# Performance work log

Hardware: AMD Instinct MI355X
Metric: run time of the kernel (lower is better)

Reference implementation:

```python
import jax, jax.numpy as jnp
import numpy as np
from jax import lax

DIM = 1024      # model dim
DS = 16         # d_state
DC = 4          # d_conv
EXP = 2
DI = DIM * EXP  # d_inner = 2048
B, L = 2, 1024


def setup_inputs() -> dict:
    key = jax.random.key(0)
    ks = jax.random.split(key, 10)
    s = lambda k, shape, sc: jax.random.normal(k, shape, jnp.float32) * sc
    return {
        "x": s(ks[0], (B, L, DIM), 1.0),
        "norm_w": jnp.ones((DIM,), jnp.float32),
        "norm_b": jnp.zeros((DIM,), jnp.float32),
        "in_proj_w": s(ks[1], (2 * DI, DIM), DIM ** -0.5),
        "conv_w": s(ks[2], (DI, 1, DC), DC ** -0.5),   # depthwise: (out=DI, in/groups=1, K)
        "conv_b": jnp.zeros((DI,), jnp.float32),
        "x_proj_w": s(ks[3], (2 * DS + 1, DI), DI ** -0.5),
        "dt_w": s(ks[4], (DI, 1), 1.0),
        "dt_b": jax.random.uniform(ks[5], (DI,), jnp.float32, -0.001, 0.001),
        "A_log": s(ks[6], (DI, DS), 1.0),              # self.A (randn); A = -exp(A_log)
        "D_skip": jnp.ones((DI,), jnp.float32),
        "out_proj_w": s(ks[7], (DIM, DI), DI ** -0.5),
    }


def _ssm(x, x_proj_w, dt_w, dt_b, A_log, D_skip):
    # x: (B, L, DI)
    xp = jnp.einsum('bli,pi->blp', x, x_proj_w)            # (B, L, 2*DS+1)
    delta = jax.nn.softplus(xp[..., :1] * dt_w[:, 0] + dt_b)  # (B, L, DI)
    Bp = xp[..., 1:DS + 1]                                  # (B, L, DS)
    Cp = xp[..., DS + 1:]                                   # (B, L, DS)
    A = -jnp.exp(A_log)                                     # (DI, DS)
    dA = jnp.exp(delta[..., None] * A)                      # (B, L, DI, DS)
    dB = delta[..., None] * Bp[:, :, None, :] * x[..., None]  # (B, L, DI, DS)

    def step(h, inp):
        dA_t, dB_t, C_t = inp                               # (B,DI,DS),(B,DI,DS),(B,DS)
        h = dA_t * h + dB_t
        return h, jnp.einsum('bdn,bn->bd', h, C_t)

    h0 = jnp.zeros((x.shape[0], DI, DS), x.dtype)
    _, ys = lax.scan(step, h0, (jnp.swapaxes(dA, 0, 1),
                                jnp.swapaxes(dB, 0, 1),
                                jnp.swapaxes(Cp, 0, 1)))
    y = jnp.swapaxes(ys, 0, 1)                              # (B, L, DI)
    return y + x * D_skip


def reference(x, norm_w, norm_b, in_proj_w, conv_w, conv_b,
              x_proj_w, dt_w, dt_b, A_log, D_skip, out_proj_w):
    # LayerNorm
    mu = x.mean(-1, keepdims=True)
    var = ((x - mu) ** 2).mean(-1, keepdims=True)
    xn = (x - mu) * lax.rsqrt(var + 1e-5) * norm_w + norm_b
    # input projection and gate split
    xz = jnp.einsum('bld,pd->blp', xn, in_proj_w)           # (B, L, 2*DI)
    xi, z = xz[..., :DI], xz[..., DI:]
    # causal depthwise conv (torch pads K-1 both sides then slices [:L] == left-pad K-1)
    xc = lax.conv_general_dilated(jnp.swapaxes(xi, 1, 2), conv_w, (1,),
                                  [(DC - 1, 0)], feature_group_count=DI,
                                  dimension_numbers=('NCH', 'OIH', 'NCH'))
    xc = jnp.swapaxes(xc + conv_b[None, :, None], 1, 2)     # (B, L, DI)
    xc = jax.nn.silu(xc)
    y = _ssm(xc, x_proj_w, dt_w, dt_b, A_log, D_skip)
    y = y * jax.nn.silu(z)
    return x + jnp.einsum('bli,di->bld', y, out_proj_w)
```

## Files before the change

kernel.cpp:

```cpp
#include <hip/hip_runtime.h>
#include <stdint.h>

#define BATCH 2
#define SEQ   1024
#define DIM_  1024
#define DS_   16
#define DI_   2048
#define NTOK  (BATCH*SEQ)
#define NSEG  32
#define LSEG  (SEQ/NSEG)

typedef unsigned short u16;
using s16x8 = __attribute__((ext_vector_type(8))) short;
using f32x4 = __attribute__((ext_vector_type(4))) float;
using u16x4 = __attribute__((ext_vector_type(4))) unsigned short;
using u16x8 = __attribute__((ext_vector_type(8))) unsigned short;

__device__ __forceinline__ float bf2f(u16 u) {
  union { unsigned int i; float f; } c; c.i = ((unsigned int)u) << 16; return c.f;
}
__device__ __forceinline__ u16 f2bf(float f) {
  union { float f; unsigned int i; } c; c.f = f;
  unsigned int r = c.i + 0x7fffu + ((c.i >> 16) & 1u);
  return (u16)(r >> 16);
}
__device__ __forceinline__ float softplus_f(float x) {
  return (x > 15.f) ? x : __logf(1.f + __expf(x));
}
__device__ __forceinline__ u16x4 f4_to_bf(float4 v) {
  u16x4 r; r[0] = f2bf(v.x); r[1] = f2bf(v.y); r[2] = f2bf(v.z); r[3] = f2bf(v.w);
  return r;
}

#define N4_INW  (2 * DI_ * DIM_ / 4)
#define N4_OUTW (DIM_ * DI_ / 4)
__global__ __launch_bounds__(256) void cvt_all_kernel(const float* __restrict__ in_w,
    const float* __restrict__ out_w, const float* __restrict__ xproj_w,
    u16* __restrict__ in_w_bf, u16* __restrict__ out_w_bf, u16* __restrict__ xpw_bf) {
  int i = blockIdx.x * 256 + threadIdx.x;
  if (i < N4_INW) {
    ((u16x4*)in_w_bf)[i] = f4_to_bf(((const float4*)in_w)[i]);
  } else if (i < N4_INW + N4_OUTW) {
    int j = i - N4_INW;
    ((u16x4*)out_w_bf)[j] = f4_to_bf(((const float4*)out_w)[j]);
  } else {
    int j = i - (N4_INW + N4_OUTW);
    if (j >= 32768) return;
    int p = (j * 4) >> 11;
    u16x4 r;
    if (p < 33) r = f4_to_bf(((const float4*)xproj_w)[j]);
    else { r[0] = 0; r[1] = 0; r[2] = 0; r[3] = 0; }
    ((u16x4*)xpw_bf)[j] = r;
  }
}

__global__ __launch_bounds__(256) void ln_kernel(const float* __restrict__ x,
    const float* __restrict__ w, const float* __restrict__ b, u16* __restrict__ xn) {
  int t = blockIdx.x, tid = threadIdx.x;
  const float* row = x + (size_t)t * DIM_;
  float4 v = ((const float4*)row)[tid];
  float f[4] = {v.x, v.y, v.z, v.w};
  float s = 0.f, sq = 0.f;
#pragma unroll
  for (int j = 0; j < 4; j++) { s += f[j]; sq += f[j] * f[j]; }
#pragma unroll
  for (int m = 1; m < 64; m <<= 1) { s += __shfl_xor(s, m); sq += __shfl_xor(sq, m); }
  __shared__ float rs_[4], rq_[4];
  int wv = tid >> 6;
  if ((tid & 63) == 0) { rs_[wv] = s; rq_[wv] = sq; }
  __syncthreads();
  s = rs_[0] + rs_[1] + rs_[2] + rs_[3];
  sq = rq_[0] + rq_[1] + rq_[2] + rq_[3];
  float mu = s * (1.0f / DIM_);
  float var = sq * (1.0f / DIM_) - mu * mu;
  float rstd = rsqrtf(var + 1e-5f);
  float4 wn = ((const float4*)w)[tid];
  float4 bn = ((const float4*)b)[tid];
  u16x4 o;
  o[0] = f2bf((f[0] - mu) * rstd * wn.x + bn.x);
  o[1] = f2bf((f[1] - mu) * rstd * wn.y + bn.y);
  o[2] = f2bf((f[2] - mu) * rstd * wn.z + bn.z);
  o[3] = f2bf((f[3] - mu) * rstd * wn.w + bn.w);
  *(u16x4*)(xn + (size_t)t * DIM_ + tid * 4) = o;
}

template<int TBM, int TBN, int BK, typename OUT, int EPI, int KSPLIT = 1, int SWZ = 0>
__global__ __launch_bounds__(256) void gemm_bt(const u16* __restrict__ A,
    const u16* __restrict__ Wt, OUT* __restrict__ C, const float* __restrict__ X,
    int M, int N, int K) {
  constexpr int LDT = BK + 8;
  constexpr int TPR = BK / 8;
  constexpr int RPP = 256 / TPR;
  constexpr int ALn = TBM / RPP;
  constexpr int BLn = TBN / RPP;
  constexpr int KK = BK / 32;
  constexpr int WM = TBM / 2, WN = TBN / 2;
  constexpr int MI = WM / 16, NJ = WN / 16;
  __shared__ __align__(16) u16 sA[TBM * LDT];
  __shared__ __align__(16) u16 sB[TBN * LDT];
  const int tid = threadIdx.x;
  const int lane = tid & 63, wv = tid >> 6;
  const int wm = (wv >> 1) * WM, wn = (wv & 1) * WN;
  const int bxl = SWZ ? ((blockIdx.x & 7) * (gridDim.x >> 3) + (blockIdx.x >> 3))
                      : blockIdx.x;
  const int bm0 = blockIdx.y * TBM, bn0 = bxl * TBN;
  const int q = lane >> 4, r16 = lane & 15;
  const int srow = tid / TPR, scol = (tid % TPR) * 8;
  const int kc = K / KSPLIT;
  const int k0 = (KSPLIT > 1) ? blockIdx.z * kc : 0;
  const int kend = k0 + kc;

  f32x4 acc[MI][NJ];
#pragma unroll
  for (int i = 0; i < MI; i++)
#pragma unroll
    for (int j = 0; j < NJ; j++)
#pragma unroll
      for (int r = 0; r < 4; r++) acc[i][j][r] = 0.f;

  const u16* Ag = A + (size_t)bm0 * K + scol + k0;
  const u16* Wg = Wt + (size_t)bn0 * K + scol + k0;
  s16x8 ra[ALn], rb[BLn];
#pragma unroll
  for (int i = 0; i < ALn; i++) ra[i] = *(const s16x8*)(Ag + (size_t)(srow + i * RPP) * K);
#pragma unroll
  for (int i = 0; i < BLn; i++) rb[i] = *(const s16x8*)(Wg + (size_t)(srow + i * RPP) * K);

  for (int kt = k0; kt < kend; kt += BK) {
    __syncthreads();
#pragma unroll
    for (int i = 0; i < ALn; i++) *(s16x8*)&sA[(srow + i * RPP) * LDT + scol] = ra[i];
#pragma unroll
    for (int i = 0; i < BLn; i++) *(s16x8*)&sB[(srow + i * RPP) * LDT + scol] = rb[i];
    __syncthreads();
    int kn = kt + BK - k0;
    if (kn < kc) {
#pragma unroll
      for (int i = 0; i < ALn; i++) ra[i] = *(const s16x8*)(Ag + (size_t)(srow + i * RPP) * K + kn);
#pragma unroll
      for (int i = 0; i < BLn; i++) rb[i] = *(const s16x8*)(Wg + (size_t)(srow + i * RPP) * K + kn);
    }
#pragma unroll
    for (int kk = 0; kk < KK; kk++) {
      s16x8 fa[MI], fb[NJ];
#pragma unroll
      for (int i = 0; i < MI; i++)
        fa[i] = *(const s16x8*)&sA[(wm + i * 16 + r16) * LDT + kk * 32 + q * 8];
#pragma unroll
      for (int j = 0; j < NJ; j++)
        fb[j] = *(const s16x8*)&sB[(wn + j * 16 + r16) * LDT + kk * 32 + q * 8];
#pragma unroll
      for (int i = 0; i < MI; i++)
#pragma unroll
        for (int j = 0; j < NJ; j++)
          acc[i][j] = __builtin_amdgcn_mfma_f32_16x16x32_bf16(fa[i], fb[j], acc[i][j], 0, 0, 0);
    }
  }
  OUT* Cz = C + ((KSPLIT > 1) ? (size_t)blockIdx.z * M * N : 0);
#pragma unroll
  for (int i = 0; i < MI; i++)
#pragma unroll
    for (int j = 0; j < NJ; j++) {
      int row0 = bm0 + wm + i * 16 + q * 4;
      int col = bn0 + wn + j * 16 + r16;
#pragma unroll
      for (int r = 0; r < 4; r++) {
        size_t off = (size_t)(row0 + r) * N + col;
        float v = acc[i][j][r];
        if constexpr (EPI == 1) v += X[off];
        if constexpr (sizeof(OUT) == 2) Cz[off] = f2bf(v);
        else                            Cz[off] = v;
      }
    }
}

__global__ __launch_bounds__(256) void conv_silu_kernel(const u16* __restrict__ xz,
    const float* __restrict__ cw, const float* __restrict__ cb, u16* __restrict__ xc) {
  int t = blockIdx.x;
  int l = t & (SEQ - 1);
  int c0 = threadIdx.x * 8;
  float acc[8], wk[8][4];
#pragma unroll
  for (int j = 0; j < 8; j++) {
    float4 wv = ((const float4*)cw)[c0 + j];
    wk[j][0] = wv.x; wk[j][1] = wv.y; wk[j][2] = wv.z; wk[j][3] = wv.w;
    acc[j] = cb[c0 + j];
  }
#pragma unroll
  for (int k = 0; k < 4; k++) {
    int lk = l - 3 + k;
    if (lk >= 0) {
      u16x8 v = *(const u16x8*)(xz + (size_t)(t - 3 + k) * (2 * DI_) + c0);
#pragma unroll
      for (int j = 0; j < 8; j++) acc[j] = fmaf(bf2f(v[j]), wk[j][k], acc[j]);
    }
  }
  u16x8 o;
#pragma unroll
  for (int j = 0; j < 8; j++) {
    float a = acc[j];
    o[j] = f2bf(a / (1.0f + __expf(-a)));
  }
  *(u16x8*)(xc + (size_t)t * DI_ + c0) = o;
}

__global__ __launch_bounds__(256) void xp_finish_kernel(const float* __restrict__ part,
    const float* __restrict__ dtw, const float* __restrict__ dtb,
    u16* __restrict__ xz, float* __restrict__ bc) {
  int t = blockIdx.x;
  int tid = threadIdx.x;
  __shared__ float xps[64];
  if (tid < 64) {
    float s = 0.f;
#pragma unroll
    for (int k = 0; k < 8; k++)
      s += part[(size_t)k * NTOK * 64 + (size_t)t * 64 + tid];
    xps[tid] = s;
  }
  __syncthreads();
  if (tid < 32) bc[(size_t)t * 32 + tid] = xps[1 + tid];
  float dr = xps[0];
  int c0 = tid * 8;
  float wv[8], bv[8];
  *(float4*)wv = ((const float4*)(dtw + c0))[0];
  *(float4*)(wv + 4) = ((const float4*)(dtw + c0))[1];
  *(float4*)bv = ((const float4*)(dtb + c0))[0];
  *(float4*)(bv + 4) = ((const float4*)(dtb + c0))[1];
  u16x8 o;
#pragma unroll
  for (int j = 0; j < 8; j++) o[j] = f2bf(softplus_f(dr * wv[j] + bv[j]));
  *(u16x8*)(xz + (size_t)t * (2 * DI_) + c0) = o;
}

__global__ __launch_bounds__(256) void scan_pass1(const float* __restrict__ bc,
    const u16* __restrict__ dlt, const u16* __restrict__ xc,
    const float* __restrict__ A_log, float* __restrict__ P, float* __restrict__ Q) {
  int tid = threadIdx.x;
  int lane = tid & 63, wv = tid >> 6;
  int nl = (lane & 3) * 4;
  int d = blockIdx.x * 64 + wv * 16 + (lane >> 2);
  int s = blockIdx.y, b = blockIdx.z;
  int t0 = b * SEQ + s * LSEG;
  float4 Ain = *(const float4*)(A_log + d * DS_ + nl);
  f32x4 Av;
  Av[0] = -__expf(Ain.x); Av[1] = -__expf(Ain.y);
  Av[2] = -__expf(Ain.z); Av[3] = -__expf(Ain.w);
  f32x4 Pv, h;
#pragma unroll
  for (int i = 0; i < 4; i++) { Pv[i] = 1.f; h[i] = 0.f; }
#pragma unroll 8
  for (int j = 0; j < LSEG; j++) {
    int t = t0 + j;
    float delta = bf2f(dlt[(size_t)t * (2 * DI_) + d]);
    float xcv = bf2f(xc[(size_t)t * DI_ + d]);
    float4 B4 = *(const float4*)(bc + (size_t)t * 32 + nl);
    float du = delta * xcv;
#pragma unroll
    for (int i = 0; i < 4; i++) {
      float a = __expf(delta * Av[i]);
      Pv[i] *= a;
      float bi = (i == 0) ? B4.x : (i == 1) ? B4.y : (i == 2) ? B4.z : B4.w;
      h[i] = fmaf(a, h[i], du * bi);
    }
  }
  size_t idx = ((size_t)((b * NSEG + s) * DI_ + d)) * 16 + nl;
  *(f32x4*)(P + idx) = Pv;
  *(f32x4*)(Q + idx) = h;
}

__global__ __launch_bounds__(256) void scan_combine(const float* __restrict__ P,
    float* __restrict__ Q) {
  int g = blockIdx.x * 256 + threadIdx.x;
  int n = g & 15, d = (g >> 4) & (DI_ - 1), b = g >> 15;
  size_t base = ((size_t)b * NSEG * DI_ + d) * 16 + n;
  constexpr size_t STR = (size_t)DI_ * 16;
  float p_[NSEG], q_[NSEG];
#pragma unroll
  for (int s = 0; s < NSEG; s++) {
    p_[s] = P[base + s * STR];
    q_[s] = Q[base + s * STR];
  }
  float hh = 0.f;
#pragma unroll
  for (int s = 0; s < NSEG; s++) {
    Q[base + s * STR] = hh;
    hh = fmaf(p_[s], hh, q_[s]);
  }
}

__global__ __launch_bounds__(256) void scan_pass2(const float* __restrict__ bc,
    const u16* __restrict__ dlt, const u16* __restrict__ xc,
    const float* __restrict__ A_log, const float* __restrict__ Dskip,
    const float* __restrict__ Hin, u16* __restrict__ yb) {
  int tid = threadIdx.x;
  int lane = tid & 63, wv = tid >> 6;
  int nl = (lane & 3) * 4;
  int d = blockIdx.x * 64 + wv * 16 + (lane >> 2);
  int s = blockIdx.y, b = blockIdx.z;
  int t0 = b * SEQ + s * LSEG;
  float4 Ain = *(const float4*)(A_log + d * DS_ + nl);
  f32x4 Av;
  Av[0] = -__expf(Ain.x); Av[1] = -__expf(Ain.y);
  Av[2] = -__expf(Ain.z); Av[3] = -__expf(Ain.w);
  float Dv = Dskip[d];
  size_t idx = ((size_t)((b * NSEG + s) * DI_ + d)) * 16 + nl;
  f32x4 h = *(const f32x4*)(Hin + idx);
#pragma unroll 8
  for (int j = 0; j < LSEG; j++) {
    int t = t0 + j;
    float delta = bf2f(dlt[(size_t)t * (2 * DI_) + d]);
    float xcv = bf2f(xc[(size_t)t * DI_ + d]);
    float4 B4 = *(const float4*)(bc + (size_t)t * 32 + nl);
    float4 C4 = *(const float4*)(bc + (size_t)t * 32 + 16 + nl);
    float du = delta * xcv;
#pragma unroll
    for (int i = 0; i < 4; i++) {
      float a = __expf(delta * Av[i]);
      float bi = (i == 0) ? B4.x : (i == 1) ? B4.y : (i == 2) ? B4.z : B4.w;
      h[i] = fmaf(a, h[i], du * bi);
    }
    float p = h[0] * C4.x;
    p = fmaf(h[1], C4.y, p);
    p = fmaf(h[2], C4.z, p);
    p = fmaf(h[3], C4.w, p);
    p += __shfl_xor(p, 1);
    p += __shfl_xor(p, 2);
    if ((lane & 3) == 0) {
      float z = bf2f(dlt[(size_t)t * (2 * DI_) + DI_ + d]);
      float sz = z / (1.0f + __expf(-z));
      yb[(size_t)t * DI_ + d] = f2bf((p + xcv * Dv) * sz);
    }
  }
}

extern "C" void kernel_launch(void* const* d_in, const int* in_sizes, int n_in,
                              void* d_out, int out_size, void* d_ws, size_t ws_size,
                              hipStream_t stream) {
  const float* x      = (const float*)d_in[0];
  const float* norm_w = (const float*)d_in[1];
  const float* norm_b = (const float*)d_in[2];
  const float* in_w   = (const float*)d_in[3];
  const float* conv_w = (const float*)d_in[4];
  const float* conv_b = (const float*)d_in[5];
  const float* xproj_w= (const float*)d_in[6];
  const float* dt_w   = (const float*)d_in[7];
  const float* dt_b   = (const float*)d_in[8];
  const float* A_log  = (const float*)d_in[9];
  const float* D_skip = (const float*)d_in[10];
  const float* out_w  = (const float*)d_in[11];
  float* out = (float*)d_out;

  char* ws = (char*)d_ws;
  size_t off = 0;
  auto alloc = [&](size_t bytes) { void* p = ws + off; off += (bytes + 255) & ~255ULL; return p; };
  u16* in_w_bf  = (u16*)alloc((size_t)2 * DI_ * DIM_ * 2);
  u16* out_w_bf = (u16*)alloc((size_t)DIM_ * DI_ * 2);
  u16* xpw_bf   = (u16*)alloc((size_t)64 * DI_ * 2);
  u16* xn       = (u16*)alloc((size_t)NTOK * DIM_ * 2);
  u16* xz       = (u16*)alloc((size_t)NTOK * 2 * DI_ * 2);
  u16* xc       = (u16*)alloc((size_t)NTOK * DI_ * 2);
  float* bc     = (float*)alloc((size_t)NTOK * 32 * 4);
  float* xp_part= (float*)alloc((size_t)8 * NTOK * 64 * 4);
  float* P      = (float*)alloc((size_t)BATCH * NSEG * DI_ * 16 * 4);
  float* Q      = (float*)alloc((size_t)BATCH * NSEG * DI_ * 16 * 4);
  u16* yb       = (u16*)alloc((size_t)NTOK * DI_ * 2);

  cvt_all_kernel<<<(N4_INW + N4_OUTW + 32768 + 255) / 256, 256, 0, stream>>>(
      in_w, out_w, xproj_w, in_w_bf, out_w_bf, xpw_bf);
  ln_kernel<<<NTOK, 256, 0, stream>>>(x, norm_w, norm_b, xn);
  gemm_bt<128, 128, 64, u16, 0, 1, 1><<<dim3((2 * DI_) / 128, NTOK / 128), 256, 0, stream>>>(
      xn, in_w_bf, xz, nullptr, NTOK, 2 * DI_, DIM_);
  conv_silu_kernel<<<NTOK, 256, 0, stream>>>(xz, conv_w, conv_b, xc);
  gemm_bt<64, 64, 32, float, 0, 8><<<dim3(1, NTOK / 64, 8), 256, 0, stream>>>(
      xc, xpw_bf, xp_part, nullptr, NTOK, 64, DI_);
  xp_finish_kernel<<<NTOK, 256, 0, stream>>>(xp_part, dt_w, dt_b, xz, bc);
  scan_pass1<<<dim3(DI_ / 64, NSEG, BATCH), 256, 0, stream>>>(bc, xz, xc, A_log, P, Q);
  scan_combine<<<BATCH * DI_ * 16 / 256, 256, 0, stream>>>(P, Q);
  scan_pass2<<<dim3(DI_ / 64, NSEG, BATCH), 256, 0, stream>>>(bc, xz, xc, A_log, D_skip,
                                                              Q, yb);
  gemm_bt<64, 64, 64, float, 1, 1, 1><<<dim3(DIM_ / 64, NTOK / 64), 256, 0, stream>>>(
      yb, out_w_bf, out, x, NTOK, DIM_, DI_);
}
```

Before: 235.5 us.

## Fuse xp-finish and three scan stages into one cooperative kernel with grid syncs

```diff
diff --git a/kernel.cpp b/kernel.cpp
--- a/kernel.cpp
+++ b/kernel.cpp
@@ -1,5 +1,8 @@
 #include <hip/hip_runtime.h>
+#include <hip/hip_cooperative_groups.h>
 #include <stdint.h>
+
+namespace cg = cooperative_groups;
 
 #define BATCH 2
 #define SEQ   1024
@@ -7,7 +10,7 @@
 #define DS_   16
 #define DI_   2048
 #define NTOK  (BATCH*SEQ)
-#define NSEG  32
+#define NSEG  16
 #define LSEG  (SEQ/NSEG)
 
 typedef unsigned short u16;
@@ -34,29 +37,32 @@
 
 #define N4_INW  (2 * DI_ * DIM_ / 4)
 #define N4_OUTW (DIM_ * DI_ / 4)
-__global__ __launch_bounds__(256) void cvt_all_kernel(const float* __restrict__ in_w,
+#define CVT_BLOCKS ((N4_INW + N4_OUTW + 32768) / 256)
+__global__ __launch_bounds__(256) void cvt_ln_kernel(const float* __restrict__ in_w,
     const float* __restrict__ out_w, const float* __restrict__ xproj_w,
-    u16* __restrict__ in_w_bf, u16* __restrict__ out_w_bf, u16* __restrict__ xpw_bf) {
-  int i = blockIdx.x * 256 + threadIdx.x;
-  if (i < N4_INW) {
-    ((u16x4*)in_w_bf)[i] = f4_to_bf(((const float4*)in_w)[i]);
-  } else if (i < N4_INW + N4_OUTW) {
-    int j = i - N4_INW;
-    ((u16x4*)out_w_bf)[j] = f4_to_bf(((const float4*)out_w)[j]);
-  } else {
-    int j = i - (N4_INW + N4_OUTW);
-    if (j >= 32768) return;
-    int p = (j * 4) >> 11;
-    u16x4 r;
-    if (p < 33) r = f4_to_bf(((const float4*)xproj_w)[j]);
-    else { r[0] = 0; r[1] = 0; r[2] = 0; r[3] = 0; }
-    ((u16x4*)xpw_bf)[j] = r;
-  }
-}
-
-__global__ __launch_bounds__(256) void ln_kernel(const float* __restrict__ x,
-    const float* __restrict__ w, const float* __restrict__ b, u16* __restrict__ xn) {
-  int t = blockIdx.x, tid = threadIdx.x;
+    const float* __restrict__ x, const float* __restrict__ nw,
+    const float* __restrict__ nb, u16* __restrict__ in_w_bf,
+    u16* __restrict__ out_w_bf, u16* __restrict__ xpw_bf, u16* __restrict__ xn) {
+  int tid = threadIdx.x;
+  if (blockIdx.x < CVT_BLOCKS) {
+    int i = blockIdx.x * 256 + tid;
+    if (i < N4_INW) {
+      ((u16x4*)in_w_bf)[i] = f4_to_bf(((const float4*)in_w)[i]);
+    } else if (i < N4_INW + N4_OUTW) {
+      int j = i - N4_INW;
+      ((u16x4*)out_w_bf)[j] = f4_to_bf(((const float4*)out_w)[j]);
+    } else {
+      int j = i - (N4_INW + N4_OUTW);
+      if (j >= 32768) return;
+      int p = (j * 4) >> 11;
+      u16x4 r;
+      if (p < 33) r = f4_to_bf(((const float4*)xproj_w)[j]);
+      else { r[0] = 0; r[1] = 0; r[2] = 0; r[3] = 0; }
+      ((u16x4*)xpw_bf)[j] = r;
+    }
+    return;
+  }
+  int t = blockIdx.x - CVT_BLOCKS;
   const float* row = x + (size_t)t * DIM_;
   float4 v = ((const float4*)row)[tid];
   float f[4] = {v.x, v.y, v.z, v.w};
@@ -74,8 +80,8 @@
   float mu = s * (1.0f / DIM_);
   float var = sq * (1.0f / DIM_) - mu * mu;
   float rstd = rsqrtf(var + 1e-5f);
-  float4 wn = ((const float4*)w)[tid];
-  float4 bn = ((const float4*)b)[tid];
+  float4 wn = ((const float4*)nw)[tid];
+  float4 bn = ((const float4*)nb)[tid];
   u16x4 o;
   o[0] = f2bf((f[0] - mu) * rstd * wn.x + bn.x);
   o[1] = f2bf((f[1] - mu) * rstd * wn.y + bn.y);
@@ -204,131 +210,128 @@
   *(u16x8*)(xc + (size_t)t * DI_ + c0) = o;
 }
 
-__global__ __launch_bounds__(256) void xp_finish_kernel(const float* __restrict__ part,
-    const float* __restrict__ dtw, const float* __restrict__ dtb,
-    u16* __restrict__ xz, float* __restrict__ bc) {
-  int t = blockIdx.x;
-  int tid = threadIdx.x;
+__global__ __launch_bounds__(256, 4) void scan_fused(
+    const float* __restrict__ part, const float* __restrict__ dtw,
+    const float* __restrict__ dtb, u16* __restrict__ xz, float* __restrict__ bc,
+    const u16* __restrict__ xc, const float* __restrict__ A_log,
+    const float* __restrict__ Dskip, float* __restrict__ P, float* __restrict__ Q,
+    u16* __restrict__ yb) {
+  cg::grid_group grid = cg::this_grid();
+  const int bid = blockIdx.x;
+  const int tid = threadIdx.x;
   __shared__ float xps[64];
-  if (tid < 64) {
-    float s = 0.f;
-#pragma unroll
-    for (int k = 0; k < 8; k++)
-      s += part[(size_t)k * NTOK * 64 + (size_t)t * 64 + tid];
-    xps[tid] = s;
-  }
-  __syncthreads();
-  if (tid < 32) bc[(size_t)t * 32 + tid] = xps[1 + tid];
-  float dr = xps[0];
-  int c0 = tid * 8;
-  float wv[8], bv[8];
-  *(float4*)wv = ((const float4*)(dtw + c0))[0];
-  *(float4*)(wv + 4) = ((const float4*)(dtw + c0))[1];
-  *(float4*)bv = ((const float4*)(dtb + c0))[0];
-  *(float4*)(bv + 4) = ((const float4*)(dtb + c0))[1];
-  u16x8 o;
-#pragma unroll
-  for (int j = 0; j < 8; j++) o[j] = f2bf(softplus_f(dr * wv[j] + bv[j]));
-  *(u16x8*)(xz + (size_t)t * (2 * DI_) + c0) = o;
-}
-
-__global__ __launch_bounds__(256) void scan_pass1(const float* __restrict__ bc,
-    const u16* __restrict__ dlt, const u16* __restrict__ xc,
-    const float* __restrict__ A_log, float* __restrict__ P, float* __restrict__ Q) {
-  int tid = threadIdx.x;
-  int lane = tid & 63, wv = tid >> 6;
-  int nl = (lane & 3) * 4;
-  int d = blockIdx.x * 64 + wv * 16 + (lane >> 2);
-  int s = blockIdx.y, b = blockIdx.z;
-  int t0 = b * SEQ + s * LSEG;
+
+  for (int tt = 0; tt < 2; tt++) {
+    int t = bid * 2 + tt;
+    if (tid < 64) {
+      float s = 0.f;
+#pragma unroll
+      for (int k = 0; k < 8; k++)
+        s += part[(size_t)k * NTOK * 64 + (size_t)t * 64 + tid];
+      xps[tid] = s;
+    }
+    __syncthreads();
+    if (tid < 32) bc[(size_t)t * 32 + tid] = xps[1 + tid];
+    float dr = xps[0];
+    int c0 = tid * 8;
+    float wv8[8], bv8[8];
+    *(float4*)wv8 = ((const float4*)(dtw + c0))[0];
+    *(float4*)(wv8 + 4) = ((const float4*)(dtw + c0))[1];
+    *(float4*)bv8 = ((const float4*)(dtb + c0))[0];
+    *(float4*)(bv8 + 4) = ((const float4*)(dtb + c0))[1];
+    u16x8 o;
+#pragma unroll
+    for (int j = 0; j < 8; j++) o[j] = f2bf(softplus_f(dr * wv8[j] + bv8[j]));
+    *(u16x8*)(xz + (size_t)t * (2 * DI_) + c0) = o;
+    __syncthreads();
+  }
+  grid.sync();
+
+  const int lane = tid & 63, wv = tid >> 6;
+  const int nl = (lane & 3) * 4;
+  const int d_blk = bid & 31, seg = (bid >> 5) & 15, b = bid >> 9;
+  const int d = d_blk * 64 + wv * 16 + (lane >> 2);
+  const int t0 = b * SEQ + seg * LSEG;
   float4 Ain = *(const float4*)(A_log + d * DS_ + nl);
   f32x4 Av;
   Av[0] = -__expf(Ain.x); Av[1] = -__expf(Ain.y);
   Av[2] = -__expf(Ain.z); Av[3] = -__expf(Ain.w);
-  f32x4 Pv, h;
-#pragma unroll
-  for (int i = 0; i < 4; i++) { Pv[i] = 1.f; h[i] = 0.f; }
-#pragma unroll 8
-  for (int j = 0; j < LSEG; j++) {
-    int t = t0 + j;
-    float delta = bf2f(dlt[(size_t)t * (2 * DI_) + d]);
-    float xcv = bf2f(xc[(size_t)t * DI_ + d]);
-    float4 B4 = *(const float4*)(bc + (size_t)t * 32 + nl);
-    float du = delta * xcv;
-#pragma unroll
-    for (int i = 0; i < 4; i++) {
-      float a = __expf(delta * Av[i]);
-      Pv[i] *= a;
-      float bi = (i == 0) ? B4.x : (i == 1) ? B4.y : (i == 2) ? B4.z : B4.w;
-      h[i] = fmaf(a, h[i], du * bi);
-    }
-  }
-  size_t idx = ((size_t)((b * NSEG + s) * DI_ + d)) * 16 + nl;
-  *(f32x4*)(P + idx) = Pv;
-  *(f32x4*)(Q + idx) = h;
-}
-
-__global__ __launch_bounds__(256) void scan_combine(const float* __restrict__ P,
-    float* __restrict__ Q) {
-  int g = blockIdx.x * 256 + threadIdx.x;
-  int n = g & 15, d = (g >> 4) & (DI_ - 1), b = g >> 15;
-  size_t base = ((size_t)b * NSEG * DI_ + d) * 16 + n;
-  constexpr size_t STR = (size_t)DI_ * 16;
-  float p_[NSEG], q_[NSEG];
-#pragma unroll
-  for (int s = 0; s < NSEG; s++) {
-    p_[s] = P[base + s * STR];
-    q_[s] = Q[base + s * STR];
-  }
-  float hh = 0.f;
-#pragma unroll
-  for (int s = 0; s < NSEG; s++) {
-    Q[base + s * STR] = hh;
-    hh = fmaf(p_[s], hh, q_[s]);
-  }
-}
-
-__global__ __launch_bounds__(256) void scan_pass2(const float* __restrict__ bc,
-    const u16* __restrict__ dlt, const u16* __restrict__ xc,
-    const float* __restrict__ A_log, const float* __restrict__ Dskip,
-    const float* __restrict__ Hin, u16* __restrict__ yb) {
-  int tid = threadIdx.x;
-  int lane = tid & 63, wv = tid >> 6;
-  int nl = (lane & 3) * 4;
-  int d = blockIdx.x * 64 + wv * 16 + (lane >> 2);
-  int s = blockIdx.y, b = blockIdx.z;
-  int t0 = b * SEQ + s * LSEG;
-  float4 Ain = *(const float4*)(A_log + d * DS_ + nl);
-  f32x4 Av;
-  Av[0] = -__expf(Ain.x); Av[1] = -__expf(Ain.y);
-  Av[2] = -__expf(Ain.z); Av[3] = -__expf(Ain.w);
-  float Dv = Dskip[d];
-  size_t idx = ((size_t)((b * NSEG + s) * DI_ + d)) * 16 + nl;
-  f32x4 h = *(const f32x4*)(Hin + idx);
-#pragma unroll 8
-  for (int j = 0; j < LSEG; j++) {
-    int t = t0 + j;
-    float delta = bf2f(dlt[(size_t)t * (2 * DI_) + d]);
-    float xcv = bf2f(xc[(size_t)t * DI_ + d]);
-    float4 B4 = *(const float4*)(bc + (size_t)t * 32 + nl);
-    float4 C4 = *(const float4*)(bc + (size_t)t * 32 + 16 + nl);
-    float du = delta * xcv;
-#pragma unroll
-    for (int i = 0; i < 4; i++) {
-      float a = __expf(delta * Av[i]);
-      float bi = (i == 0) ? B4.x : (i == 1) ? B4.y : (i == 2) ? B4.z : B4.w;
-      h[i] = fmaf(a, h[i], du * bi);
-    }
-    float p = h[0] * C4.x;
-    p = fmaf(h[1], C4.y, p);
-    p = fmaf(h[2], C4.z, p);
-    p = fmaf(h[3], C4.w, p);
-    p += __shfl_xor(p, 1);
-    p += __shfl_xor(p, 2);
-    if ((lane & 3) == 0) {
-      float z = bf2f(dlt[(size_t)t * (2 * DI_) + DI_ + d]);
-      float sz = z / (1.0f + __expf(-z));
-      yb[(size_t)t * DI_ + d] = f2bf((p + xcv * Dv) * sz);
+  const size_t idx = ((size_t)((b * NSEG + seg) * DI_ + d)) * 16 + nl;
+
+  {
+    f32x4 Pv, h;
+#pragma unroll
+    for (int i = 0; i < 4; i++) { Pv[i] = 1.f; h[i] = 0.f; }
+#pragma unroll 4
+    for (int j = 0; j < LSEG; j++) {
+      int t = t0 + j;
+      float delta = bf2f(xz[(size_t)t * (2 * DI_) + d]);
+      float xcv = bf2f(xc[(size_t)t * DI_ + d]);
+      float4 B4 = *(const float4*)(bc + (size_t)t * 32 + nl);
+      float du = delta * xcv;
+#pragma unroll
+      for (int i = 0; i < 4; i++) {
+        float a = __expf(delta * Av[i]);
+        Pv[i] *= a;
+        float bi = (i == 0) ? B4.x : (i == 1) ? B4.y : (i == 2) ? B4.z : B4.w;
+        h[i] = fmaf(a, h[i], du * bi);
+      }
+    }
+    *(f32x4*)(P + idx) = Pv;
+    *(f32x4*)(Q + idx) = h;
+  }
+  grid.sync();
+
+  {
+    int g = bid * 256 + tid;
+    if (g < BATCH * DI_ * 16) {
+      int n2 = g & 15, d2 = (g >> 4) & (DI_ - 1), b2 = g >> 15;
+      size_t base = ((size_t)b2 * NSEG * DI_ + d2) * 16 + n2;
+      constexpr size_t STR = (size_t)DI_ * 16;
+      float p_[NSEG], q_[NSEG];
+#pragma unroll
+      for (int s = 0; s < NSEG; s++) {
+        p_[s] = P[base + s * STR];
+        q_[s] = Q[base + s * STR];
+      }
+      float hh = 0.f;
+#pragma unroll
+      for (int s = 0; s < NSEG; s++) {
+        Q[base + s * STR] = hh;
+        hh = fmaf(p_[s], hh, q_[s]);
+      }
+    }
+  }
+  grid.sync();
+
+  {
+    float Dv = Dskip[d];
+    f32x4 h = *(const f32x4*)(Q + idx);
+#pragma unroll 4
+    for (int j = 0; j < LSEG; j++) {
+      int t = t0 + j;
+      float delta = bf2f(xz[(size_t)t * (2 * DI_) + d]);
+      float xcv = bf2f(xc[(size_t)t * DI_ + d]);
+      float4 B4 = *(const float4*)(bc + (size_t)t * 32 + nl);
+      float4 C4 = *(const float4*)(bc + (size_t)t * 32 + 16 + nl);
+      float du = delta * xcv;
+#pragma unroll
+      for (int i = 0; i < 4; i++) {
+        float a = __expf(delta * Av[i]);
+        float bi = (i == 0) ? B4.x : (i == 1) ? B4.y : (i == 2) ? B4.z : B4.w;
+        h[i] = fmaf(a, h[i], du * bi);
+      }
+      float p = h[0] * C4.x;
+      p = fmaf(h[1], C4.y, p);
+      p = fmaf(h[2], C4.z, p);
+      p = fmaf(h[3], C4.w, p);
+      p += __shfl_xor(p, 1);
+      p += __shfl_xor(p, 2);
+      if ((lane & 3) == 0) {
+        float z = bf2f(xz[(size_t)t * (2 * DI_) + DI_ + d]);
+        float sz = z / (1.0f + __expf(-z));
+        yb[(size_t)t * DI_ + d] = f2bf((p + xcv * Dv) * sz);
+      }
     }
   }
 }
@@ -365,19 +368,21 @@
   float* Q      = (float*)alloc((size_t)BATCH * NSEG * DI_ * 16 * 4);
   u16* yb       = (u16*)alloc((size_t)NTOK * DI_ * 2);
 
-  cvt_all_kernel<<<(N4_INW + N4_OUTW + 32768 + 255) / 256, 256, 0, stream>>>(
-      in_w, out_w, xproj_w, in_w_bf, out_w_bf, xpw_bf);
-  ln_kernel<<<NTOK, 256, 0, stream>>>(x, norm_w, norm_b, xn);
+  cvt_ln_kernel<<<CVT_BLOCKS + NTOK, 256, 0, stream>>>(in_w, out_w, xproj_w, x,
+                                                       norm_w, norm_b, in_w_bf,
+                                                       out_w_bf, xpw_bf, xn);
   gemm_bt<128, 128, 64, u16, 0, 1, 1><<<dim3((2 * DI_) / 128, NTOK / 128), 256, 0, stream>>>(
       xn, in_w_bf, xz, nullptr, NTOK, 2 * DI_, DIM_);
   conv_silu_kernel<<<NTOK, 256, 0, stream>>>(xz, conv_w, conv_b, xc);
   gemm_bt<64, 64, 32, float, 0, 8><<<dim3(1, NTOK / 64, 8), 256, 0, stream>>>(
       xc, xpw_bf, xp_part, nullptr, NTOK, 64, DI_);
-  xp_finish_kernel<<<NTOK, 256, 0, stream>>>(xp_part, dt_w, dt_b, xz, bc);
-  scan_pass1<<<dim3(DI_ / 64, NSEG, BATCH), 256, 0, stream>>>(bc, xz, xc, A_log, P, Q);
-  scan_combine<<<BATCH * DI_ * 16 / 256, 256, 0, stream>>>(P, Q);
-  scan_pass2<<<dim3(DI_ / 64, NSEG, BATCH), 256, 0, stream>>>(bc, xz, xc, A_log, D_skip,
-                                                              Q, yb);
+  {
+    void* args[] = {(void*)&xp_part, (void*)&dt_w, (void*)&dt_b, (void*)&xz,
+                    (void*)&bc, (void*)&xc, (void*)&A_log, (void*)&D_skip,
+                    (void*)&P, (void*)&Q, (void*)&yb};
+    hipLaunchCooperativeKernel((const void*)scan_fused, dim3(1024), dim3(256),
+                               args, 0, stream);
+  }
   gemm_bt<64, 64, 64, float, 1, 1, 1><<<dim3(DIM_ / 64, NTOK / 64), 256, 0, stream>>>(
       yb, out_w_bf, out, x, NTOK, DIM_, DI_);
 }
```

New measurement: 550.6 us. +133.8%, slower.
